# Kernel tuning notes

Hardware: AMD Instinct MI355X
Metric: run time of the kernel (lower is better)

## Reference

```python
import jax, jax.numpy as jnp
import numpy as np

HEAD_DIM = 64
EMBED_DIM = 1024

def setup_inputs() -> dict:
    key = jax.random.key(0)
    k1, k2, k3, k4 = jax.random.split(key, 4)
    x = jax.random.normal(k1, (4, 4096, EMBED_DIM), dtype=jnp.float32)
    # nn.Linear(embed_dim, head_dim, bias=False): weight shape (head_dim, embed_dim)
    s = 1.0 / np.sqrt(EMBED_DIM)
    Wq = jax.random.uniform(k2, (HEAD_DIM, EMBED_DIM), jnp.float32, -s, s)
    Wk = jax.random.uniform(k3, (HEAD_DIM, EMBED_DIM), jnp.float32, -s, s)
    Wv = jax.random.uniform(k4, (HEAD_DIM, EMBED_DIM), jnp.float32, -s, s)
    return {"x": x, "Wq": Wq, "Wk": Wk, "Wv": Wv}

def reference(x, Wq, Wk, Wv):
    # Faithful to source: V = self.key(x), i.e. uses Wk (Wv is an unused param).
    n_ctx = x.shape[1]
    Q = jnp.einsum('bse,de->bsd', x, Wq)
    K = jnp.einsum('bse,de->bsd', x, Wk)
    V = jnp.einsum('bse,de->bsd', x, Wk)
    scale = 1.0 / jnp.sqrt(jnp.asarray(K.shape[-1], x.dtype))
    scores = jnp.einsum('bqd,bkd->bqk', Q, K) * scale  # [b, n_ctx, n_ctx]
    causal = jnp.tril(jnp.ones((n_ctx, n_ctx), dtype=bool))
    scores = jnp.where(causal, scores, jnp.asarray(-jnp.inf, scores.dtype))
    attn = jax.nn.softmax(scores, axis=-1)
    # dropout(p=0.2) omitted: reference runs in eval mode (identity)
    out = jnp.einsum('bqk,bkd->bqd', attn, V)
    return out
```

## Files before the change

kernel.cpp:

```cpp
#include <hip/hip_runtime.h>

typedef _Float16 f16;
typedef _Float16 f16x8 __attribute__((ext_vector_type(8)));
typedef _Float16 f16x4 __attribute__((ext_vector_type(4)));
typedef float f32x4 __attribute__((ext_vector_type(4)));

#define S_LEN 4096
#define B_SZ  4
#define E_DIM 1024
#define D_DIM 64
#define NROWS (B_SZ * S_LEN)
#define NSPLIT 4
#define QSCALE (0.125f * 1.44269504088896f)
#define SMAX 8.0f

__device__ __forceinline__ float exp2g(float x) { return __builtin_amdgcn_exp2f(x); }

__global__ __launch_bounds__(256) void wpack_kernel(const float* __restrict__ Wq,
                                                    const float* __restrict__ Wk,
                                                    f16* __restrict__ Bp) {
    int id = blockIdx.x * 256 + threadIdx.x;
    int lane = id & 63, kc = (id >> 6) & 31, n = id >> 11;
    int row = n * 16 + (lane & 15);
    int col = kc * 32 + (lane >> 4) * 8;
    const float* src = (row < 64) ? (Wq + (long)row * E_DIM + col)
                                  : (Wk + (long)(row - 64) * E_DIM + col);
    float4 v0 = ((const float4*)src)[0];
    float4 v1 = ((const float4*)src)[1];
    f16x8 h = {(f16)v0.x, (f16)v0.y, (f16)v0.z, (f16)v0.w,
               (f16)v1.x, (f16)v1.y, (f16)v1.z, (f16)v1.w};
    *(f16x8*)(Bp + (long)id * 8) = h;
}

__global__ __launch_bounds__(256, 2) void proj_kernel(const float* __restrict__ x,
                                                      const f16* __restrict__ Bp,
                                                      f16* __restrict__ Qh,
                                                      f16* __restrict__ Kh) {
    __shared__ union {
        f16 xs[32][1032];
        f16 os[32][136];
    } sm;

    const int tid  = threadIdx.x;
    const int w    = tid >> 6;
    const int lane = tid & 63;
    const int l15  = lane & 15;
    const int quad = lane >> 4;
    const long m0  = (long)blockIdx.x * 32;

#pragma unroll
    for (int c = 0; c < 16; c++) {
        int f8 = c * 256 + tid;
        int row = f8 >> 7;
        int col = (f8 & 127) * 8;
        const float* src = x + (m0 + row) * E_DIM + col;
        float4 v0 = ((const float4*)src)[0];
        float4 v1 = ((const float4*)src)[1];
        f16x8 h = {(f16)v0.x, (f16)v0.y, (f16)v0.z, (f16)v0.w,
                   (f16)v1.x, (f16)v1.y, (f16)v1.z, (f16)v1.w};
        *(f16x8*)&sm.xs[row][col] = h;
    }
    __syncthreads();

    f32x4 acc[2][2];
#pragma unroll
    for (int m = 0; m < 2; m++)
#pragma unroll
        for (int nn = 0; nn < 2; nn++) acc[m][nn] = (f32x4){0.f, 0.f, 0.f, 0.f};

    const int n0 = w * 2;
#pragma unroll 4
    for (int kc = 0; kc < 32; kc++) {
        f16x8 a0 = *(const f16x8*)&sm.xs[l15][kc * 32 + quad * 8];
        f16x8 a1 = *(const f16x8*)&sm.xs[16 + l15][kc * 32 + quad * 8];
#pragma unroll
        for (int nn = 0; nn < 2; nn++) {
            f16x8 b = *(const f16x8*)(Bp + (((long)(n0 + nn) * 32 + kc) * 64 + lane) * 8);
            acc[0][nn] = __builtin_amdgcn_mfma_f32_16x16x32_f16(a0, b, acc[0][nn], 0, 0, 0);
            acc[1][nn] = __builtin_amdgcn_mfma_f32_16x16x32_f16(a1, b, acc[1][nn], 0, 0, 0);
        }
    }
    __syncthreads();

#pragma unroll
    for (int m = 0; m < 2; m++)
#pragma unroll
        for (int nn = 0; nn < 2; nn++) {
            int colg = w * 32 + nn * 16 + l15;
            float sc = (colg < 64) ? QSCALE : 1.0f;
#pragma unroll
            for (int r = 0; r < 4; r++)
                sm.os[m * 16 + quad * 4 + r][colg] = (f16)(acc[m][nn][r] * sc);
        }
    __syncthreads();

    {
        int row = tid >> 3, cg = tid & 7;
        long grow = m0 + row;
#pragma unroll
        for (int h = 0; h < 2; h++) {
            int col = cg * 16 + h * 8;
            f16x8 v = *(const f16x8*)&sm.os[row][col];
            if (col < 64) *(f16x8*)(Qh + grow * 64 + col)        = v;
            else          *(f16x8*)(Kh + grow * 64 + (col - 64)) = v;
        }
    }
}

__global__ __launch_bounds__(256, 2) void attn_kernel(const f16* __restrict__ Qh,
                                                      const f16* __restrict__ Kh,
                                                      float* __restrict__ OutP0,
                                                      f16* __restrict__ P123,
                                                      float* __restrict__ Ml) {
    __shared__ __align__(16) f16 Kr[2][64][72];
    __shared__ __align__(16) f16 Kt[2][64][72];
    __shared__ __align__(16) f16 Pm[128][88];

    const int tid  = threadIdx.x;
    const int w    = tid >> 6;
    const int lane = tid & 63;
    const int l15  = lane & 15;
    const int quad = lane >> 4;

    const int bid  = blockIdx.x;
    const int b    = bid & 3;
    const int half = (bid >> 2) & 3;
    const int qraw = bid >> 4;
    const int qt   = 31 - qraw;
    const long q0  = (long)qt * 128;
    const int jmax = 2 * qt + 1;

    const f16* Qb = Qh + (long)b * S_LEN * 64;
    const f16* Kb = Kh + (long)b * S_LEN * 64;

    f16x8 Aq[2][2];
#pragma unroll
    for (int m = 0; m < 2; m++)
#pragma unroll
        for (int kf = 0; kf < 2; kf++)
            Aq[m][kf] = *(const f16x8*)(Qb + (q0 + w * 32 + m * 16 + l15) * 64 + kf * 32 + quad * 8);

    const f16x8 ones = {(f16)1.f, (f16)1.f, (f16)1.f, (f16)1.f,
                        (f16)1.f, (f16)1.f, (f16)1.f, (f16)1.f};

    f32x4 O[2][4];
    f32x4 Lacc[2];
#pragma unroll
    for (int m = 0; m < 2; m++) {
        Lacc[m] = (f32x4){0.f, 0.f, 0.f, 0.f};
#pragma unroll
        for (int n = 0; n < 4; n++) O[m][n] = (f32x4){0.f, 0.f, 0.f, 0.f};
    }

    f16x8 pre[2];
    if (half <= jmax) {
#pragma unroll
        for (int it = 0; it < 2; it++)
            pre[it] = *(const f16x8*)(Kb + ((long)half * 64 + lane) * 64 + (w + it * 4) * 8);
    }

    int buf = 0;
    for (int j = half; j <= jmax; j += NSPLIT) {
#pragma unroll
        for (int it = 0; it < 2; it++) {
            int sg = w + it * 4;
            *(f16x8*)&Kr[buf][lane][sg * 8] = pre[it];
#pragma unroll
            for (int i = 0; i < 8; i++) Kt[buf][sg * 8 + i][lane] = pre[it][i];
        }
        if (j + NSPLIT <= jmax) {
#pragma unroll
            for (int it = 0; it < 2; it++)
                pre[it] = *(const f16x8*)(Kb + ((long)(j + NSPLIT) * 64 + lane) * 64 + (w + it * 4) * 8);
        }
        __syncthreads();

        const int odiag = j * 64 - (int)q0;
        const bool alive = !(odiag == 64 && w < 2);
        if (alive) {
            f32x4 S[2][4];
#pragma unroll
            for (int m = 0; m < 2; m++)
#pragma unroll
                for (int n = 0; n < 4; n++) S[m][n] = (f32x4){0.f, 0.f, 0.f, 0.f};

            __builtin_amdgcn_s_setprio(1);
#pragma unroll
            for (int n = 0; n < 4; n++)
#pragma unroll
                for (int kf = 0; kf < 2; kf++) {
                    f16x8 bfr = *(const f16x8*)&Kr[buf][n * 16 + l15][kf * 32 + quad * 8];
                    S[0][n] = __builtin_amdgcn_mfma_f32_16x16x32_f16(Aq[0][kf], bfr, S[0][n], 0, 0, 0);
                    S[1][n] = __builtin_amdgcn_mfma_f32_16x16x32_f16(Aq[1][kf], bfr, S[1][n], 0, 0, 0);
                }
            __builtin_amdgcn_s_setprio(0);

            if (odiag >= 0) {
#pragma unroll
                for (int m = 0; m < 2; m++) {
                    int rbase = w * 32 + m * 16 + quad * 4;
#pragma unroll
                    for (int n = 0; n < 4; n++) {
                        int colrel = odiag + n * 16 + l15;
#pragma unroll
                        for (int r = 0; r < 4; r++)
                            if (colrel > rbase + r) S[m][n][r] = -1e30f;
                    }
                }
            }

#pragma unroll
            for (int m = 0; m < 2; m++)
#pragma unroll
                for (int n = 0; n < 4; n++)
#pragma unroll
                    for (int r = 0; r < 4; r++)
                        Pm[w * 32 + m * 16 + quad * 4 + r][n * 16 + l15] =
                            (f16)exp2g(S[m][n][r] - SMAX);

            __builtin_amdgcn_s_setprio(1);
#pragma unroll
            for (int kf = 0; kf < 2; kf++) {
                f16x8 pa0 = *(const f16x8*)&Pm[w * 32 + l15][kf * 32 + quad * 8];
                f16x8 pa1 = *(const f16x8*)&Pm[w * 32 + 16 + l15][kf * 32 + quad * 8];
                Lacc[0] = __builtin_amdgcn_mfma_f32_16x16x32_f16(pa0, ones, Lacc[0], 0, 0, 0);
                Lacc[1] = __builtin_amdgcn_mfma_f32_16x16x32_f16(pa1, ones, Lacc[1], 0, 0, 0);
#pragma unroll
                for (int n = 0; n < 4; n++) {
                    f16x8 vb = *(const f16x8*)&Kt[buf][n * 16 + l15][kf * 32 + quad * 8];
                    O[0][n] = __builtin_amdgcn_mfma_f32_16x16x32_f16(pa0, vb, O[0][n], 0, 0, 0);
                    O[1][n] = __builtin_amdgcn_mfma_f32_16x16x32_f16(pa1, vb, O[1][n], 0, 0, 0);
                }
            }
            __builtin_amdgcn_s_setprio(0);
        }
        buf ^= 1;
    }

    const long growbase = (long)b * S_LEN + q0;
#pragma unroll
    for (int m = 0; m < 2; m++)
#pragma unroll
        for (int r = 0; r < 4; r++) {
            long grow = growbase + w * 32 + m * 16 + quad * 4 + r;
            if (half == 0) {
#pragma unroll
                for (int n = 0; n < 4; n++) OutP0[grow * 64 + n * 16 + l15] = O[m][n][r];
            } else {
                f16* dst = P123 + (long)(half - 1) * NROWS * 64;
#pragma unroll
                for (int n = 0; n < 4; n++) dst[grow * 64 + n * 16 + l15] = (f16)O[m][n][r];
            }
            if (l15 == 0) Ml[(long)half * NROWS + grow] = Lacc[m][r];
        }
}

__global__ __launch_bounds__(256) void combine_kernel(float* __restrict__ Out,
                                                      const f16* __restrict__ P123,
                                                      const float* __restrict__ Ml) {
    int gid = blockIdx.x * 256 + threadIdx.x;
    long row = gid >> 4;
    int c0 = (gid & 15) * 4;
    float lt = 0.f;
#pragma unroll
    for (int h = 0; h < 4; h++) lt += Ml[(long)h * NROWS + row];
    float inv = 1.0f / lt;

    float* p = Out + row * 64 + c0;
    float4 res = *(const float4*)p;
#pragma unroll
    for (int h = 1; h < 4; h++) {
        f16x4 oh = *(const f16x4*)(P123 + (long)(h - 1) * NROWS * 64 + row * 64 + c0);
        res.x += (float)oh[0];
        res.y += (float)oh[1];
        res.z += (float)oh[2];
        res.w += (float)oh[3];
    }
    *(float4*)p = make_float4(res.x * inv, res.y * inv, res.z * inv, res.w * inv);
}

extern "C" void kernel_launch(void* const* d_in, const int* in_sizes, int n_in,
                              void* d_out, int out_size, void* d_ws, size_t ws_size,
                              hipStream_t stream) {
    const float* x  = (const float*)d_in[0];
    const float* Wq = (const float*)d_in[1];
    const float* Wk = (const float*)d_in[2];
    float* out = (float*)d_out;

    f16* Qh    = (f16*)d_ws;
    f16* Kh    = Qh + (long)NROWS * D_DIM;
    f16* Bp    = Kh + (long)NROWS * D_DIM;
    f16* P123  = Bp + (long)128 * E_DIM;
    float* Ml  = (float*)(P123 + 3L * NROWS * D_DIM);

    wpack_kernel<<<dim3(64), dim3(256), 0, stream>>>(Wq, Wk, Bp);
    proj_kernel<<<dim3(NROWS / 32), dim3(256), 0, stream>>>(x, Bp, Qh, Kh);
    attn_kernel<<<dim3(32 * NSPLIT * B_SZ), dim3(256), 0, stream>>>(Qh, Kh, out, P123, Ml);
    combine_kernel<<<dim3(NROWS * 16 / 256), dim3(256), 0, stream>>>(out, P123, Ml);
}
```

Measured before the change: 131.6 us.

## Compute transposed scores with 32x32 MFMA and keep P in registers

The attention kernel now computes S^T = K·Q^T with 32x32x16 MFMAs so each lane holds a query column. The exponentiated probabilities are packed to f16 and rearranged with permlane32_swap into the A-operand layout for the PV MFMA, which removes the shared-memory Pm round trip and its stores and loads. Row sums are taken with fdot2 instead of an MFMA against ones, and fully masked warps skip more precisely. The query-tile order also alternates between large and small tiles to balance load. The cost is more register pressure from the 16-wide accumulators, plus extra permute and conversion instructions.

Result: faster. 126.0 us (-4.3%).

```diff
diff --git a/kernel.cpp b/kernel.cpp
--- a/kernel.cpp
+++ b/kernel.cpp
@@ -3,7 +3,10 @@
 typedef _Float16 f16;
 typedef _Float16 f16x8 __attribute__((ext_vector_type(8)));
 typedef _Float16 f16x4 __attribute__((ext_vector_type(4)));
+typedef __fp16 h2 __attribute__((ext_vector_type(2)));
 typedef float f32x4 __attribute__((ext_vector_type(4)));
+typedef float f32x16 __attribute__((ext_vector_type(16)));
+typedef unsigned u32x2 __attribute__((ext_vector_type(2)));
 
 #define S_LEN 4096
 #define B_SZ  4
@@ -114,43 +117,32 @@
                                                       float* __restrict__ Ml) {
     __shared__ __align__(16) f16 Kr[2][64][72];
     __shared__ __align__(16) f16 Kt[2][64][72];
-    __shared__ __align__(16) f16 Pm[128][88];
 
     const int tid  = threadIdx.x;
     const int w    = tid >> 6;
     const int lane = tid & 63;
-    const int l15  = lane & 15;
-    const int quad = lane >> 4;
+    const int l31  = lane & 31;
+    const int hi   = lane >> 5;
 
     const int bid  = blockIdx.x;
     const int b    = bid & 3;
     const int half = (bid >> 2) & 3;
     const int qraw = bid >> 4;
-    const int qt   = 31 - qraw;
-    const long q0  = (long)qt * 128;
+    const int qt   = (qraw < 16) ? (31 - qraw) : (qraw - 16);
+    const int q0i  = qt * 128;
+    const long q0  = (long)q0i;
     const int jmax = 2 * qt + 1;
 
     const f16* Qb = Qh + (long)b * S_LEN * 64;
     const f16* Kb = Kh + (long)b * S_LEN * 64;
 
-    f16x8 Aq[2][2];
-#pragma unroll
-    for (int m = 0; m < 2; m++)
-#pragma unroll
-        for (int kf = 0; kf < 2; kf++)
-            Aq[m][kf] = *(const f16x8*)(Qb + (q0 + w * 32 + m * 16 + l15) * 64 + kf * 32 + quad * 8);
-
-    const f16x8 ones = {(f16)1.f, (f16)1.f, (f16)1.f, (f16)1.f,
-                        (f16)1.f, (f16)1.f, (f16)1.f, (f16)1.f};
-
-    f32x4 O[2][4];
-    f32x4 Lacc[2];
-#pragma unroll
-    for (int m = 0; m < 2; m++) {
-        Lacc[m] = (f32x4){0.f, 0.f, 0.f, 0.f};
-#pragma unroll
-        for (int n = 0; n < 4; n++) O[m][n] = (f32x4){0.f, 0.f, 0.f, 0.f};
-    }
+    f16x8 Bq[4];
+#pragma unroll
+    for (int kf = 0; kf < 4; kf++)
+        Bq[kf] = *(const f16x8*)(Qb + (q0 + w * 32 + l31) * 64 + kf * 16 + hi * 8);
+
+    f32x16 O0 = {}, O1 = {};
+    float Lc[4] = {0.f, 0.f, 0.f, 0.f};
 
     f16x8 pre[2];
     if (half <= jmax) {
@@ -175,84 +167,102 @@
         }
         __syncthreads();
 
-        const int odiag = j * 64 - (int)q0;
-        const bool alive = !(odiag == 64 && w < 2);
+        const int od = j * 64 - q0i;
+        const bool alive = (od <= w * 32 + 31);
         if (alive) {
-            f32x4 S[2][4];
-#pragma unroll
-            for (int m = 0; m < 2; m++)
-#pragma unroll
-                for (int n = 0; n < 4; n++) S[m][n] = (f32x4){0.f, 0.f, 0.f, 0.f};
-
+            f32x16 Sc0 = {}, Sc1 = {};
             __builtin_amdgcn_s_setprio(1);
 #pragma unroll
-            for (int n = 0; n < 4; n++)
-#pragma unroll
-                for (int kf = 0; kf < 2; kf++) {
-                    f16x8 bfr = *(const f16x8*)&Kr[buf][n * 16 + l15][kf * 32 + quad * 8];
-                    S[0][n] = __builtin_amdgcn_mfma_f32_16x16x32_f16(Aq[0][kf], bfr, S[0][n], 0, 0, 0);
-                    S[1][n] = __builtin_amdgcn_mfma_f32_16x16x32_f16(Aq[1][kf], bfr, S[1][n], 0, 0, 0);
+            for (int kf = 0; kf < 4; kf++) {
+                f16x8 a0 = *(const f16x8*)&Kr[buf][l31][kf * 16 + hi * 8];
+                f16x8 a1 = *(const f16x8*)&Kr[buf][32 + l31][kf * 16 + hi * 8];
+                Sc0 = __builtin_amdgcn_mfma_f32_32x32x16_f16(a0, Bq[kf], Sc0, 0, 0, 0);
+                Sc1 = __builtin_amdgcn_mfma_f32_32x32x16_f16(a1, Bq[kf], Sc1, 0, 0, 0);
+            }
+            __builtin_amdgcn_s_setprio(0);
+
+            if (od + 63 > w * 32) {
+                const int thr = w * 32 + l31 - od - 4 * hi;
+#pragma unroll
+                for (int r = 0; r < 16; r++) {
+                    const int rc = (r & 3) + 8 * (r >> 2);
+                    if (rc > thr)      Sc0[r] = -1e30f;
+                    if (rc + 32 > thr) Sc1[r] = -1e30f;
                 }
+            }
+
+            f32x16 pe0, pe1;
+#pragma unroll
+            for (int r = 0; r < 16; r++) {
+                pe0[r] = exp2g(Sc0[r] - SMAX);
+                pe1[r] = exp2g(Sc1[r] - SMAX);
+            }
+
+            unsigned Cw[8][2];
+#pragma unroll
+            for (int u = 0; u < 8; u++) {
+#pragma unroll
+                for (int cp = 0; cp < 2; cp++) {
+                    const int e = 4 * (u & 3) + 2 * cp;
+                    h2 t = (u < 4) ? __builtin_amdgcn_cvt_pkrtz(pe0[e], pe0[e + 1])
+                                   : __builtin_amdgcn_cvt_pkrtz(pe1[e], pe1[e + 1]);
+                    Cw[u][cp] = __builtin_bit_cast(unsigned, t);
+                }
+            }
+
+            h2 one2;
+            one2[0] = (__fp16)1.f;
+            one2[1] = (__fp16)1.f;
+#pragma unroll
+            for (int u = 0; u < 8; u++)
+#pragma unroll
+                for (int cp = 0; cp < 2; cp++) {
+                    const int c = (u & 1) * 2 + cp;
+                    Lc[c] = __builtin_amdgcn_fdot2(__builtin_bit_cast(h2, Cw[u][cp]),
+                                                   one2, Lc[c], false);
+                }
+
+            f16x8 pa[4];
+#pragma unroll
+            for (int kc = 0; kc < 4; kc++) {
+                u32x2 s0 = __builtin_amdgcn_permlane32_swap(Cw[2 * kc][0], Cw[2 * kc + 1][0], false, false);
+                u32x2 s1 = __builtin_amdgcn_permlane32_swap(Cw[2 * kc][1], Cw[2 * kc + 1][1], false, false);
+                union { unsigned uw[4]; f16x8 v; } pw;
+                pw.uw[0] = s0.x; pw.uw[1] = s1.x; pw.uw[2] = s0.y; pw.uw[3] = s1.y;
+                pa[kc] = pw.v;
+            }
+
+            __builtin_amdgcn_s_setprio(1);
+#pragma unroll
+            for (int kc = 0; kc < 4; kc++) {
+                f16x8 v0 = *(const f16x8*)&Kt[buf][l31][kc * 16 + hi * 8];
+                f16x8 v1 = *(const f16x8*)&Kt[buf][32 + l31][kc * 16 + hi * 8];
+                O0 = __builtin_amdgcn_mfma_f32_32x32x16_f16(pa[kc], v0, O0, 0, 0, 0);
+                O1 = __builtin_amdgcn_mfma_f32_32x32x16_f16(pa[kc], v1, O1, 0, 0, 0);
+            }
             __builtin_amdgcn_s_setprio(0);
-
-            if (odiag >= 0) {
-#pragma unroll
-                for (int m = 0; m < 2; m++) {
-                    int rbase = w * 32 + m * 16 + quad * 4;
-#pragma unroll
-                    for (int n = 0; n < 4; n++) {
-                        int colrel = odiag + n * 16 + l15;
-#pragma unroll
-                        for (int r = 0; r < 4; r++)
-                            if (colrel > rbase + r) S[m][n][r] = -1e30f;
-                    }
-                }
-            }
-
-#pragma unroll
-            for (int m = 0; m < 2; m++)
-#pragma unroll
-                for (int n = 0; n < 4; n++)
-#pragma unroll
-                    for (int r = 0; r < 4; r++)
-                        Pm[w * 32 + m * 16 + quad * 4 + r][n * 16 + l15] =
-                            (f16)exp2g(S[m][n][r] - SMAX);
-
-            __builtin_amdgcn_s_setprio(1);
-#pragma unroll
-            for (int kf = 0; kf < 2; kf++) {
-                f16x8 pa0 = *(const f16x8*)&Pm[w * 32 + l15][kf * 32 + quad * 8];
-                f16x8 pa1 = *(const f16x8*)&Pm[w * 32 + 16 + l15][kf * 32 + quad * 8];
-                Lacc[0] = __builtin_amdgcn_mfma_f32_16x16x32_f16(pa0, ones, Lacc[0], 0, 0, 0);
-                Lacc[1] = __builtin_amdgcn_mfma_f32_16x16x32_f16(pa1, ones, Lacc[1], 0, 0, 0);
-#pragma unroll
-                for (int n = 0; n < 4; n++) {
-                    f16x8 vb = *(const f16x8*)&Kt[buf][n * 16 + l15][kf * 32 + quad * 8];
-                    O[0][n] = __builtin_amdgcn_mfma_f32_16x16x32_f16(pa0, vb, O[0][n], 0, 0, 0);
-                    O[1][n] = __builtin_amdgcn_mfma_f32_16x16x32_f16(pa1, vb, O[1][n], 0, 0, 0);
-                }
-            }
-            __builtin_amdgcn_s_setprio(0);
         }
         buf ^= 1;
     }
 
+    float Lt = Lc[0] + Lc[1] + Lc[2] + Lc[3];
+    Lt += __shfl_xor(Lt, 32, 64);
+
     const long growbase = (long)b * S_LEN + q0;
 #pragma unroll
-    for (int m = 0; m < 2; m++)
-#pragma unroll
-        for (int r = 0; r < 4; r++) {
-            long grow = growbase + w * 32 + m * 16 + quad * 4 + r;
-            if (half == 0) {
-#pragma unroll
-                for (int n = 0; n < 4; n++) OutP0[grow * 64 + n * 16 + l15] = O[m][n][r];
-            } else {
-                f16* dst = P123 + (long)(half - 1) * NROWS * 64;
-#pragma unroll
-                for (int n = 0; n < 4; n++) dst[grow * 64 + n * 16 + l15] = (f16)O[m][n][r];
-            }
-            if (l15 == 0) Ml[(long)half * NROWS + grow] = Lacc[m][r];
-        }
+    for (int r = 0; r < 16; r++) {
+        const int rc = (r & 3) + 8 * (r >> 2);
+        long grow = growbase + w * 32 + rc + 4 * hi;
+        if (half == 0) {
+            OutP0[grow * 64 + l31]      = O0[r];
+            OutP0[grow * 64 + 32 + l31] = O1[r];
+        } else {
+            f16* dst = P123 + (long)(half - 1) * NROWS * 64;
+            dst[grow * 64 + l31]      = (f16)O0[r];
+            dst[grow * 64 + 32 + l31] = (f16)O1[r];
+        }
+    }
+    if (hi == 0) Ml[(long)half * NROWS + growbase + w * 32 + l31] = Lt;
 }
 
 __global__ __launch_bounds__(256) void combine_kernel(float* __restrict__ Out,
```
